# Kernel tuning notes

Hardware: AMD Instinct MI355X
Metric: run time of the kernel (lower is better)

## Reference

```python
import jax, jax.numpy as jnp
import numpy as np

EARTH_R_MILES = 3958.8
NEG_INF = -1e30  # finite sentinel; exp underflows to 0 exactly

def haversine(lat1, lon1, lat2, lon2):
    lat1, lon1 = jnp.deg2rad(lat1), jnp.deg2rad(lon1)
    lat2, lon2 = jnp.deg2rad(lat2), jnp.deg2rad(lon2)
    dlat = lat2 - lat1
    dlon = lon2 - lon1
    a = jnp.sin(dlat / 2) ** 2 + jnp.cos(lat1) * jnp.cos(lat2) * jnp.sin(dlon / 2) ** 2
    c = 2.0 * jnp.arctan2(jnp.sqrt(a), jnp.sqrt(1.0 - a))
    return EARTH_R_MILES * c

def setup_inputs() -> dict:
    key = jax.random.key(0)
    k1, k2, k3, k4 = jax.random.split(key, 4)
    B, NBINS, M = 8192, 125, 4096
    preds_lonlat = jax.random.normal(k1, (B, 2), dtype=jnp.float32) * 10.0
    # candidate [lon, lat] coords per bin, padded to M
    bin_coords = jax.random.uniform(k2, (NBINS, M, 2), dtype=jnp.float32) * 10.0
    # three categorical columns, each in [0, 5)
    x_vals = jax.random.randint(k3, (B, 3), 0, 5, dtype=jnp.int64)
    # ragged bin sizes in [1, M] (non-empty; original skips empty bins)
    bin_counts = jax.random.randint(k4, (NBINS,), 1, M + 1, dtype=jnp.int64)
    return {"preds_lonlat": preds_lonlat, "bin_coords": bin_coords,
            "x_vals": x_vals, "bin_counts": bin_counts}

def reference(preds_lonlat, bin_coords, x_vals, bin_counts):
    tau = 0.25
    M = bin_coords.shape[1]
    # flat bin id from categorical key (5 categories per column)
    bin_ids = x_vals[:, 0] * 25 + x_vals[:, 1] * 5 + x_vals[:, 2]      # [B]
    cand = bin_coords[bin_ids]                                          # [B, M, 2] (lon, lat)
    counts = bin_counts[bin_ids]                                        # [B]
    mask = jnp.arange(M)[None, :] < counts[:, None]                     # [B, M]
    lon_p = preds_lonlat[:, 0:1]                                        # [B, 1]
    lat_p = preds_lonlat[:, 1:2]
    dists = haversine(lat_p, lon_p, cand[..., 1], cand[..., 0])         # [B, M]
    logits = jnp.where(mask, -dists / tau, NEG_INF)
    soft_min = -tau * jax.scipy.special.logsumexp(logits, axis=1)       # [B]
    valid = counts > 0
    n_valid = jnp.maximum(jnp.sum(valid), 1)
    loss = jnp.sum(jnp.where(valid, soft_min, 0.0)) / n_valid
    return loss
```

## Files before the change

kernel.cpp:

```cpp
#include <hip/hip_runtime.h>
#include <math.h>

#define D2R      0.017453292519943295f
#define TWO_R    7917.6f
#define RPI2     12435.698f
#define TAU_LN2  0.17328679513998632f
#define K_EXP2   5.770780163555854f
#define MBIG     1.0e30f
#define DMASK    2.0e30f
#define NBINS    125
#define P        8

__device__ __forceinline__ float fexp2(float x) { return __builtin_amdgcn_exp2f(x); }
__device__ __forceinline__ float rfl(float x) {
  return __int_as_float(__builtin_amdgcn_readfirstlane(__float_as_int(x)));
}

struct Ws {
  float accF;
  int   accI;
  int   nitems;
  int   pad;
  int   pbase[NBINS];
  int   pcnt[NBINS];
  int   work[4096];
};
#define PTRIG_OFF 17408

__global__ __launch_bounds__(1024) void group_kernel(
    const float2* __restrict__ preds, const int* __restrict__ xv,
    Ws* __restrict__ w, int B) {
  __shared__ int lcnt[NBINS], lbase[NBINS], lcur[NBINS], lg[NBINS];
  const int tid = threadIdx.x;

  for (int b = tid; b < NBINS; b += 1024) lcnt[b] = 0;
  __syncthreads();

  for (int i = tid; i < B; i += 1024) {
    int bin = xv[3 * i] * 25 + xv[3 * i + 1] * 5 + xv[3 * i + 2];
    atomicAdd(&lcnt[bin], 1);
  }
  __syncthreads();

  if (tid == 0) {
    int base = 0, gtot = 0;
    for (int b = 0; b < NBINS; ++b) {
      lbase[b] = base; base += lcnt[b];
      lg[b]    = gtot; gtot += (lcnt[b] + P - 1) / P;
    }
    w->nitems = gtot;
  }
  __syncthreads();

  for (int b = tid; b < NBINS; b += 1024) {
    lcur[b]     = lbase[b];
    w->pbase[b] = lbase[b];
    w->pcnt[b]  = lcnt[b];
    int g0 = lg[b], ng = (lcnt[b] + P - 1) / P;
    for (int g = 0; g < ng; ++g) w->work[g0 + g] = (b << 16) | g;
  }
  __syncthreads();

  float4* ptrig = (float4*)((char*)w + PTRIG_OFF);
  for (int i = tid; i < B; i += 1024) {
    int bin = xv[3 * i] * 25 + xv[3 * i + 1] * 5 + xv[3 * i + 2];
    int pos = atomicAdd(&lcur[bin], 1);
    float2 p = preds[i];
    float sA, cA, sO, cO;
    __sincosf(p.y * D2R, &sA, &cA);
    __sincosf(p.x * D2R, &sO, &cO);
    ptrig[pos] = make_float4(cA, sA, cO, sO);
  }
}

__global__ __launch_bounds__(256) void lse_main(
    const float2* __restrict__ bc, const int* __restrict__ bin_counts,
    Ws* __restrict__ w, int M) {
  const int nitems = w->nitems;
  const int bid = blockIdx.x;
  if (bid >= nitems) return;
  const int tid = threadIdx.x;

  const int item   = w->work[bid];
  const int bin    = item >> 16;
  const int g      = item & 0xffff;
  const int npred  = w->pcnt[bin];
  const int pb     = w->pbase[bin] + g * P;
  const int pcount = min(P, npred - g * P);
  const int cnt    = bin_counts[bin];

  const float4* __restrict__ ptrig = (const float4*)((const char*)w + PTRIG_OFF);

  float cA[P], sA[P], cO[P], sO[P];
#pragma unroll
  for (int p = 0; p < P; ++p) {
    float4 t = ptrig[pb + min(p, pcount - 1)];
    cA[p] = rfl(t.x); sA[p] = rfl(t.y); cO[p] = rfl(t.z); sO[p] = rfl(t.w);
  }

  const float2* __restrict__ cb = bc + (size_t)bin * (size_t)M;
  const int cmax   = cnt - 1;
  const int nsteps = (cnt + 255) >> 8;

  float m[P], s[P];
#pragma unroll
  for (int p = 0; p < P; ++p) { m[p] = MBIG; s[p] = 0.0f; }

  float2 cur = cb[min(tid, cmax)];
  for (int step = 0; step < nsteps; ++step) {
    const int idx = (step << 8) + tid;
    float2 nxt = cb[min(idx + 256, cmax)];
    float sla, cla, slo, clo;
    __sincosf(cur.y * D2R, &sla, &cla);
    __sincosf(cur.x * D2R, &slo, &clo);
    const bool valid = idx < cnt;
#pragma unroll
    for (int p = 0; p < P; ++p) {
      float pp    = cA[p] * cla;
      float cdlat = fmaf(sA[p], sla, pp);
      float cdlon = fmaf(cO[p], clo, sO[p] * slo);
      float t1 = fmaf(-0.5f, cdlat, 0.5f);
      float t2 = fmaf(-0.5f, cdlon, 0.5f);
      float a  = fminf(fmaxf(fmaf(pp, t2, t1), 0.0f), 1.0f);
      float x  = sqrtf(a);
      float pl = fmaf(x, -0.0012624911f, 0.0066700901f);
      pl = fmaf(x, pl, -0.0170881256f);
      pl = fmaf(x, pl,  0.0308918810f);
      pl = fmaf(x, pl, -0.0501743046f);
      pl = fmaf(x, pl,  0.0889789874f);
      pl = fmaf(x, pl, -0.2145988016f);
      pl = fmaf(x, pl,  1.5707963050f);
      float wq = sqrtf(1.0f - x);
      float d  = fmaf(-TWO_R, wq * pl, RPI2);
      d = valid ? d : DMASK;
      float mn = fminf(m[p], d);
      s[p] = fmaf(s[p], fexp2((mn - m[p]) * K_EXP2), fexp2((mn - d) * K_EXP2));
      m[p] = mn;
    }
    cur = nxt;
  }

#pragma unroll
  for (int p = 0; p < P; ++p) {
#pragma unroll
    for (int o = 32; o; o >>= 1) {
      float mo = __shfl_xor(m[p], o);
      float so = __shfl_xor(s[p], o);
      float mn = fminf(m[p], mo);
      s[p] = fmaf(s[p], fexp2((mn - m[p]) * K_EXP2),
                  so * fexp2((mn - mo) * K_EXP2));
      m[p] = mn;
    }
  }

  __shared__ float redm[4][P], reds[4][P], lsoft[P];
  const int wave = tid >> 6;
  if ((tid & 63) == 0) {
#pragma unroll
    for (int p = 0; p < P; ++p) { redm[wave][p] = m[p]; reds[wave][p] = s[p]; }
  }
  __syncthreads();

  if (tid < P) {
    const int p = tid;
    float M4 = fminf(fminf(redm[0][p], redm[1][p]),
                     fminf(redm[2][p], redm[3][p]));
    float S  = reds[0][p] * fexp2((M4 - redm[0][p]) * K_EXP2)
             + reds[1][p] * fexp2((M4 - redm[1][p]) * K_EXP2)
             + reds[2][p] * fexp2((M4 - redm[2][p]) * K_EXP2)
             + reds[3][p] * fexp2((M4 - redm[3][p]) * K_EXP2);
    lsoft[p] = M4 - TAU_LN2 * __log2f(S);
  }
  __syncthreads();

  if (tid == 0 && cnt > 0) {
    float acc = 0.0f;
    for (int p = 0; p < pcount; ++p) acc += lsoft[p];
    atomicAdd(&w->accF, acc);
    atomicAdd(&w->accI, pcount);
  }
}

__global__ void fin_kernel(const Ws* __restrict__ w, float* __restrict__ out) {
  int nv = w->accI;
  if (nv < 1) nv = 1;
  out[0] = w->accF / (float)nv;
}

extern "C" void kernel_launch(void* const* d_in, const int* in_sizes, int n_in,
                              void* d_out, int out_size, void* d_ws, size_t ws_size,
                              hipStream_t stream) {
  const float2* preds      = (const float2*)d_in[0];
  const float2* bin_coords = (const float2*)d_in[1];
  const int*    x_vals     = (const int*)d_in[2];
  const int*    bin_counts = (const int*)d_in[3];
  float*        out        = (float*)d_out;

  const int B     = in_sizes[0] / 2;
  const int total = in_sizes[1] / 2;
  const int M     = total / NBINS;

  Ws* w = (Ws*)d_ws;

  hipMemsetAsync(d_ws, 0, 16, stream);

  group_kernel<<<1, 1024, 0, stream>>>(preds, x_vals, w, B);

  const int maxitems = (B + P - 1) / P + NBINS;
  lse_main<<<maxitems, 256, 0, stream>>>(bin_coords, bin_counts, w, M);

  fin_kernel<<<1, 1, 0, stream>>>(w, out);
}
```

Measured before the change: 134.8 us.

## Split candidate axis into chunks and parallelize grouping across blocks

Each prediction group's candidate loop is split into up to four 1024-candidate chunks, each handled by its own block. Partial max/sum pairs are written to workspace and combined by a new merge kernel. The single-block grouping kernel is replaced by multi-block histogram, scan and scatter kernels using global atomics. The warp reduction now takes a min pass then a sum pass. The aim is better load balance and more blocks in flight, at the cost of extra launches and more workspace traffic.

```diff
diff --git a/kernel.cpp b/kernel.cpp
--- a/kernel.cpp
+++ b/kernel.cpp
@@ -10,110 +10,114 @@
 #define DMASK    2.0e30f
 #define NBINS    125
 #define P        8
+#define CH       1024
+#define MAXCH    4
+#define NG_MAX   1152
 
 __device__ __forceinline__ float fexp2(float x) { return __builtin_amdgcn_exp2f(x); }
 __device__ __forceinline__ float rfl(float x) {
   return __int_as_float(__builtin_amdgcn_readfirstlane(__float_as_int(x)));
 }
 
-struct Ws {
-  float accF;
-  int   accI;
-  int   nitems;
-  int   pad;
-  int   pbase[NBINS];
-  int   pcnt[NBINS];
-  int   work[4096];
-};
-#define PTRIG_OFF 17408
-
-__global__ __launch_bounds__(1024) void group_kernel(
+#define W_ACCF(w)   ((float*)(w))
+#define W_ACCI(w)   ((int*)((char*)(w) + 4))
+#define W_NG(w)     ((int*)((char*)(w) + 8))
+#define W_HIST(w)   ((int*)((char*)(w) + 16))
+#define W_CUR(w)    ((int*)((char*)(w) + 528))
+#define W_PBASE(w)  ((int*)((char*)(w) + 1040))
+#define W_WREC(w)   ((int4*)((char*)(w) + 1552))
+#define W_PTRIG(w)  ((float4*)((char*)(w) + 19984))
+#define W_PM(w)     ((float*)((char*)(w) + 151056))
+#define W_PS(w)     ((float*)((char*)(w) + 298512))
+
+__global__ __launch_bounds__(256) void g1_hist(
+    const int* __restrict__ xv, void* __restrict__ w, int B) {
+  int i = blockIdx.x * 256 + threadIdx.x;
+  if (i < B) {
+    int bin = xv[3 * i] * 25 + xv[3 * i + 1] * 5 + xv[3 * i + 2];
+    atomicAdd(&W_HIST(w)[bin], 1);
+  }
+}
+
+__global__ __launch_bounds__(128) void g2_scan(
+    const int* __restrict__ bin_counts, void* __restrict__ w) {
+  __shared__ int h[NBINS], cc[NBINS], pb[NBINS], gb[NBINS];
+  const int t = threadIdx.x;
+  if (t < NBINS) { h[t] = W_HIST(w)[t]; cc[t] = bin_counts[t]; }
+  __syncthreads();
+  if (t == 0) {
+    int base = 0, g = 0;
+    for (int b = 0; b < NBINS; ++b) {
+      pb[b] = base; base += h[b];
+      gb[b] = g;    g += (h[b] + P - 1) / P;
+    }
+    *W_NG(w) = g;
+  }
+  __syncthreads();
+  if (t < NBINS) {
+    W_PBASE(w)[t] = pb[t];
+    int ng = (h[t] + P - 1) / P, g0 = gb[t], cnt = cc[t];
+    for (int g = 0; g < ng; ++g) {
+      int pbp = (pb[t] + g * P) | (min(P, h[t] - g * P) << 20);
+      W_WREC(w)[g0 + g] = make_int4(t, pbp, cnt, g);
+    }
+  }
+}
+
+__global__ __launch_bounds__(256) void g3_scatter(
     const float2* __restrict__ preds, const int* __restrict__ xv,
-    Ws* __restrict__ w, int B) {
-  __shared__ int lcnt[NBINS], lbase[NBINS], lcur[NBINS], lg[NBINS];
-  const int tid = threadIdx.x;
-
-  for (int b = tid; b < NBINS; b += 1024) lcnt[b] = 0;
-  __syncthreads();
-
-  for (int i = tid; i < B; i += 1024) {
+    void* __restrict__ w, int B) {
+  int i = blockIdx.x * 256 + threadIdx.x;
+  if (i < B) {
     int bin = xv[3 * i] * 25 + xv[3 * i + 1] * 5 + xv[3 * i + 2];
-    atomicAdd(&lcnt[bin], 1);
-  }
-  __syncthreads();
-
-  if (tid == 0) {
-    int base = 0, gtot = 0;
-    for (int b = 0; b < NBINS; ++b) {
-      lbase[b] = base; base += lcnt[b];
-      lg[b]    = gtot; gtot += (lcnt[b] + P - 1) / P;
-    }
-    w->nitems = gtot;
-  }
-  __syncthreads();
-
-  for (int b = tid; b < NBINS; b += 1024) {
-    lcur[b]     = lbase[b];
-    w->pbase[b] = lbase[b];
-    w->pcnt[b]  = lcnt[b];
-    int g0 = lg[b], ng = (lcnt[b] + P - 1) / P;
-    for (int g = 0; g < ng; ++g) w->work[g0 + g] = (b << 16) | g;
-  }
-  __syncthreads();
-
-  float4* ptrig = (float4*)((char*)w + PTRIG_OFF);
-  for (int i = tid; i < B; i += 1024) {
-    int bin = xv[3 * i] * 25 + xv[3 * i + 1] * 5 + xv[3 * i + 2];
-    int pos = atomicAdd(&lcur[bin], 1);
+    int pos = W_PBASE(w)[bin] + atomicAdd(&W_CUR(w)[bin], 1);
     float2 p = preds[i];
     float sA, cA, sO, cO;
     __sincosf(p.y * D2R, &sA, &cA);
     __sincosf(p.x * D2R, &sO, &cO);
-    ptrig[pos] = make_float4(cA, sA, cO, sO);
+    W_PTRIG(w)[pos] = make_float4(cA, sA, cO, sO);
   }
 }
 
 __global__ __launch_bounds__(256) void lse_main(
-    const float2* __restrict__ bc, const int* __restrict__ bin_counts,
-    Ws* __restrict__ w, int M) {
-  const int nitems = w->nitems;
-  const int bid = blockIdx.x;
-  if (bid >= nitems) return;
+    const float2* __restrict__ bc, void* __restrict__ w, int M) {
+  const int gi = blockIdx.x >> 2;
+  if (gi >= *W_NG(w)) return;
+  const int c = blockIdx.x & 3;
+
+  const int4 rec = W_WREC(w)[gi];
+  const int bin = rec.x, cnt = rec.z;
+  const int nch = (cnt + CH - 1) >> 10;
+  if (c >= nch) return;
+  const int pb = rec.y & 0xFFFFF;
   const int tid = threadIdx.x;
 
-  const int item   = w->work[bid];
-  const int bin    = item >> 16;
-  const int g      = item & 0xffff;
-  const int npred  = w->pcnt[bin];
-  const int pb     = w->pbase[bin] + g * P;
-  const int pcount = min(P, npred - g * P);
-  const int cnt    = bin_counts[bin];
-
-  const float4* __restrict__ ptrig = (const float4*)((const char*)w + PTRIG_OFF);
-
+  const float4* __restrict__ ptrig = W_PTRIG(w);
+  const int pcm1 = (rec.y >> 20) - 1;
   float cA[P], sA[P], cO[P], sO[P];
 #pragma unroll
   for (int p = 0; p < P; ++p) {
-    float4 t = ptrig[pb + min(p, pcount - 1)];
+    float4 t = ptrig[pb + min(p, pcm1)];
     cA[p] = rfl(t.x); sA[p] = rfl(t.y); cO[p] = rfl(t.z); sO[p] = rfl(t.w);
   }
 
   const float2* __restrict__ cb = bc + (size_t)bin * (size_t)M;
-  const int cmax   = cnt - 1;
-  const int nsteps = (cnt + 255) >> 8;
+  const int c0 = c << 10;
+  const int cend = min(cnt, c0 + CH);
+  const int nst = (cend - c0 + 255) >> 8;
 
   float m[P], s[P];
 #pragma unroll
   for (int p = 0; p < P; ++p) { m[p] = MBIG; s[p] = 0.0f; }
 
-  float2 cur = cb[min(tid, cmax)];
-  for (int step = 0; step < nsteps; ++step) {
-    const int idx = (step << 8) + tid;
-    float2 nxt = cb[min(idx + 256, cmax)];
+  float2 cur = cb[min(c0 + tid, cend - 1)];
+  for (int st = 0; st < nst; ++st) {
+    const int idx = c0 + (st << 8) + tid;
+    float2 nxt = cb[min(idx + 256, cend - 1)];
     float sla, cla, slo, clo;
     __sincosf(cur.y * D2R, &sla, &cla);
     __sincosf(cur.x * D2R, &slo, &clo);
-    const bool valid = idx < cnt;
+    const bool valid = idx < cend;
 #pragma unroll
     for (int p = 0; p < P; ++p) {
       float pp    = cA[p] * cla;
@@ -142,49 +146,70 @@
 
 #pragma unroll
   for (int p = 0; p < P; ++p) {
-#pragma unroll
-    for (int o = 32; o; o >>= 1) {
-      float mo = __shfl_xor(m[p], o);
-      float so = __shfl_xor(s[p], o);
-      float mn = fminf(m[p], mo);
-      s[p] = fmaf(s[p], fexp2((mn - m[p]) * K_EXP2),
-                  so * fexp2((mn - mo) * K_EXP2));
-      m[p] = mn;
-    }
-  }
-
-  __shared__ float redm[4][P], reds[4][P], lsoft[P];
+    float mw = m[p];
+#pragma unroll
+    for (int o = 32; o; o >>= 1) mw = fminf(mw, __shfl_xor(mw, o));
+    float sp = s[p] * fexp2((mw - m[p]) * K_EXP2);
+#pragma unroll
+    for (int o = 32; o; o >>= 1) sp += __shfl_xor(sp, o);
+    m[p] = mw; s[p] = sp;
+  }
+
+  __shared__ float redm[4][P], reds[4][P];
   const int wave = tid >> 6;
   if ((tid & 63) == 0) {
 #pragma unroll
     for (int p = 0; p < P; ++p) { redm[wave][p] = m[p]; reds[wave][p] = s[p]; }
   }
   __syncthreads();
-
   if (tid < P) {
-    const int p = tid;
-    float M4 = fminf(fminf(redm[0][p], redm[1][p]),
-                     fminf(redm[2][p], redm[3][p]));
-    float S  = reds[0][p] * fexp2((M4 - redm[0][p]) * K_EXP2)
-             + reds[1][p] * fexp2((M4 - redm[1][p]) * K_EXP2)
-             + reds[2][p] * fexp2((M4 - redm[2][p]) * K_EXP2)
-             + reds[3][p] * fexp2((M4 - redm[3][p]) * K_EXP2);
-    lsoft[p] = M4 - TAU_LN2 * __log2f(S);
-  }
-  __syncthreads();
-
-  if (tid == 0 && cnt > 0) {
-    float acc = 0.0f;
-    for (int p = 0; p < pcount; ++p) acc += lsoft[p];
-    atomicAdd(&w->accF, acc);
-    atomicAdd(&w->accI, pcount);
-  }
-}
-
-__global__ void fin_kernel(const Ws* __restrict__ w, float* __restrict__ out) {
-  int nv = w->accI;
+    float M4 = fminf(fminf(redm[0][tid], redm[1][tid]),
+                     fminf(redm[2][tid], redm[3][tid]));
+    float S4 = reds[0][tid] * fexp2((M4 - redm[0][tid]) * K_EXP2)
+             + reds[1][tid] * fexp2((M4 - redm[1][tid]) * K_EXP2)
+             + reds[2][tid] * fexp2((M4 - redm[2][tid]) * K_EXP2)
+             + reds[3][tid] * fexp2((M4 - redm[3][tid]) * K_EXP2);
+    W_PM(w)[gi * 32 + (c << 3) + tid] = M4;
+    W_PS(w)[gi * 32 + (c << 3) + tid] = S4;
+  }
+}
+
+__global__ __launch_bounds__(64) void merge_kernel(void* __restrict__ w) {
+  const int gi = blockIdx.x;
+  if (gi >= *W_NG(w)) return;
+  const int4 rec = W_WREC(w)[gi];
+  const int cnt = rec.z;
+  if (cnt <= 0) return;
+  const int nch = (cnt + CH - 1) >> 10;
+  const int pcount = rec.y >> 20;
+  const int p = threadIdx.x;
+
+  float soft = 0.0f;
+  if (p < P) {
+    float m = W_PM(w)[gi * 32 + p];
+    float s = W_PS(w)[gi * 32 + p];
+    for (int c = 1; c < nch; ++c) {
+      float mo = W_PM(w)[gi * 32 + (c << 3) + p];
+      float so = W_PS(w)[gi * 32 + (c << 3) + p];
+      float mn = fminf(m, mo);
+      s = fmaf(s, fexp2((mn - m) * K_EXP2), so * fexp2((mn - mo) * K_EXP2));
+      m = mn;
+    }
+    float val = m - TAU_LN2 * __log2f(s);
+    soft = (p < pcount) ? val : 0.0f;
+  }
+#pragma unroll
+  for (int o = 32; o; o >>= 1) soft += __shfl_xor(soft, o);
+  if (p == 0) {
+    atomicAdd(W_ACCF(w), soft);
+    atomicAdd(W_ACCI(w), pcount);
+  }
+}
+
+__global__ void fin_kernel(const void* __restrict__ w, float* __restrict__ out) {
+  int nv = *W_ACCI((void*)w);
   if (nv < 1) nv = 1;
-  out[0] = w->accF / (float)nv;
+  out[0] = *W_ACCF((void*)w) / (float)nv;
 }
 
 extern "C" void kernel_launch(void* const* d_in, const int* in_sizes, int n_in,
@@ -196,18 +221,18 @@
   const int*    bin_counts = (const int*)d_in[3];
   float*        out        = (float*)d_out;
 
-  const int B     = in_sizes[0] / 2;
-  const int total = in_sizes[1] / 2;
-  const int M     = total / NBINS;
-
-  Ws* w = (Ws*)d_ws;
-
-  hipMemsetAsync(d_ws, 0, 16, stream);
-
-  group_kernel<<<1, 1024, 0, stream>>>(preds, x_vals, w, B);
-
-  const int maxitems = (B + P - 1) / P + NBINS;
-  lse_main<<<maxitems, 256, 0, stream>>>(bin_coords, bin_counts, w, M);
-
-  fin_kernel<<<1, 1, 0, stream>>>(w, out);
-}
+  const int B = in_sizes[0] / 2;
+  const int M = (in_sizes[1] / 2) / NBINS;
+
+  hipMemsetAsync(d_ws, 0, 1040, stream);
+
+  const int pblk = (B + 255) / 256;
+  g1_hist<<<pblk, 256, 0, stream>>>(x_vals, d_ws, B);
+  g2_scan<<<1, 128, 0, stream>>>(bin_counts, d_ws);
+  g3_scatter<<<pblk, 256, 0, stream>>>(preds, x_vals, d_ws, B);
+
+  lse_main<<<NG_MAX * MAXCH, 256, 0, stream>>>(bin_coords, d_ws, M);
+
+  merge_kernel<<<NG_MAX, 64, 0, stream>>>(d_ws);
+  fin_kernel<<<1, 1, 0, stream>>>(d_ws, out);
+}
```

After: 167.9 us. +24.6%, slower.
